# Kernel optimization log

Hardware: AMD Instinct MI355X
Metric: run time of the kernel (lower is better)

Reference implementation:

```python
import jax, jax.numpy as jnp
import numpy as np

C, H = 256, 256  # feat_num, feat_h (equirect is H x 2H)


def setup_inputs() -> dict:
    key = jax.random.key(0)
    ks = jax.random.split(key, 6)
    m = jax.random.normal(ks[0], (1, C, H, 2 * H), jnp.float32)
    b = jax.random.normal(ks[1], (1, C, H, H), jnp.float32)
    u = jax.random.normal(ks[2], (1, C, H, H), jnp.float32)
    d = jax.random.normal(ks[3], (1, C, H, H), jnp.float32)
    Wf = jax.random.normal(ks[4], (C, C, 3, 3), jnp.float32) * 0.02
    bf = jnp.zeros((C,), jnp.float32)
    Wm = jax.random.normal(ks[5], (1, 2 * C, 1, 1), jnp.float32) * 0.02
    bm = jnp.zeros((1,), jnp.float32)
    return {"m": m, "b": b, "u": u, "d": d, "Wf": Wf, "bf": bf, "Wm": Wm, "bm": bm}


def _cube2equi(cube, out_h, out_w):
    # cube: [6, C, h, h]; face order: 0 back(z-), 1 down(y-), 2 front(z+), 3 left(x-), 4 right(x+), 5 up(y+)
    h = cube.shape[-1]
    theta = (jnp.arange(out_w, dtype=cube.dtype) + 0.5) / out_w * (2.0 * jnp.pi) - jnp.pi  # longitude [-pi, pi)
    phi = jnp.pi / 2 - (jnp.arange(out_h, dtype=cube.dtype) + 0.5) / out_h * jnp.pi        # latitude [pi/2, -pi/2]
    st, ct = jnp.sin(theta)[None, :], jnp.cos(theta)[None, :]
    sp, cp = jnp.sin(phi)[:, None], jnp.cos(phi)[:, None]
    dx = cp * st
    dy = jnp.broadcast_to(sp, (out_h, out_w))
    dz = cp * ct
    ax, ay, az = jnp.abs(dx), jnp.abs(dy), jnp.abs(dz)
    mx = jnp.maximum(jnp.maximum(ax, ay), az)
    px, py, pz = dx / mx, dy / mx, dz / mx
    cond_z = (az >= ax) & (az >= ay)
    cond_x = (~cond_z) & (ax >= ay)
    face = jnp.where(cond_z, jnp.where(dz > 0, 2, 0),
           jnp.where(cond_x, jnp.where(dx > 0, 4, 3),
                              jnp.where(dy > 0, 5, 1)))
    a = jnp.where(cond_z, jnp.where(dz > 0, px, -px),
        jnp.where(cond_x, jnp.where(dx > 0, -pz, pz), px))
    bcoord = jnp.where(cond_z | cond_x, -py, jnp.where(dy > 0, pz, -pz))
    uu = jnp.clip((a + 1.0) * 0.5 * (h - 1), 0.0, h - 1)
    vv = jnp.clip((bcoord + 1.0) * 0.5 * (h - 1), 0.0, h - 1)
    u0 = jnp.floor(uu).astype(jnp.int32); v0 = jnp.floor(vv).astype(jnp.int32)
    u1 = jnp.minimum(u0 + 1, h - 1); v1 = jnp.minimum(v0 + 1, h - 1)
    wu = uu - u0; wv = vv - v0

    def samp(vi, ui):
        return cube[face, :, vi, ui]  # [out_h, out_w, C] gather over all channels

    out = (samp(v0, u0) * ((1 - wv) * (1 - wu))[..., None]
         + samp(v0, u1) * ((1 - wv) * wu)[..., None]
         + samp(v1, u0) * (wv * (1 - wu))[..., None]
         + samp(v1, u1) * (wv * wu)[..., None])
    return jnp.transpose(out, (2, 0, 1))  # [C, out_h, out_w]


def _conv(x, w, bias, pad):
    y = jax.lax.conv_general_dilated(x, w, (1, 1), [(pad, pad), (pad, pad)],
                                     dimension_numbers=("NCHW", "OIHW", "NCHW"))
    return y + bias[None, :, None, None]


def reference(m, b, u, d, Wf, bf, Wm, bm):
    h = b.shape[-1]
    empty = jnp.zeros_like(b[0])  # the torch module's zero 'emptyFace' parameter
    # faces stacked as [back, down, empty, empty, empty, up], vectorized over all channels
    cube = jnp.stack([b[0], d[0], empty, empty, empty, u[0]])  # [6, C, h, h]
    aux = _cube2equi(cube, h, 2 * h)[None]                      # [1, C, h, 2h]
    M_aux = jax.nn.relu(_conv(aux, Wf, bf, 1))
    M_main = jax.nn.relu(_conv(m, Wf, bf, 1))
    mask = jax.nn.sigmoid(_conv(jnp.concatenate([M_main, M_aux], axis=1), Wm, bm, 0))
    return m + mask * M_aux
```

## Files before the change

### kernel.cpp

```cpp
#include <hip/hip_runtime.h>
#include <hip/hip_bf16.h>

#define NPIX 131072
#define WP   514
#define XP_BYTES 67897344
#define XP_STRIDE 67962880
#define FT_BYTES 100663296

typedef __attribute__((ext_vector_type(8))) short bf16x8;
typedef __attribute__((ext_vector_type(4))) float f32x4;

typedef const __attribute__((address_space(1))) void g_cvoid;
typedef __attribute__((address_space(3))) void l_void;

__device__ __forceinline__ void async16(const void* g, void* l) {
  __builtin_amdgcn_global_load_lds((g_cvoid*)g, (l_void*)l, 16, 0, 0);
}

__global__ void zero_borders(__hip_bfloat16* Xm, __hip_bfloat16* Xa) {
  int i = blockIdx.x;
  __hip_bfloat16* X = blockIdx.y ? Xa : Xm;
  long ppix;
  if (i < 514)       ppix = i;
  else if (i < 1028) ppix = 257L * WP + (i - 514);
  else if (i < 1284) ppix = (long)(i - 1028 + 1) * WP;
  else               ppix = (long)(i - 1284 + 1) * WP + 513;
  ((unsigned int*)(X + ppix * 256))[threadIdx.x] = 0u;
}

__global__ void zero_mask(float* maskacc) {
  maskacc[blockIdx.x * 256 + threadIdx.x] = 0.f;
}

__global__ void prep_weights(const float* __restrict__ Wf, __hip_bfloat16* __restrict__ Wtt) {
  int idx = blockIdx.x * 256 + threadIdx.x;
  int cout = idx / 2304, rem = idx % 2304;
  int o = rem >> 8, ci = rem & 255;
  Wtt[(((o << 5) + (ci >> 3)) << 11) + (cout << 3) + (ci & 7)] =
      __float2bfloat16(Wf[(cout * 256 + ci) * 9 + o]);
}

__global__ void nchw_to_pad_nhwc(const float* __restrict__ src, __hip_bfloat16* __restrict__ Xp) {
  __shared__ __align__(16) __hip_bfloat16 tile[64 * 264];
  int tid = threadIdx.x;
  int p0 = blockIdx.x * 64;
  int px = tid & 63, w = tid >> 6;
  for (int k = 0; k < 64; ++k) {
    int c = (k << 2) + w;
    tile[px * 264 + c] = __float2bfloat16(src[(long)c * NPIX + p0 + px]);
  }
  __syncthreads();
  int y = p0 >> 9, x0 = p0 & 511;
  long basep = (long)(y + 1) * WP + x0 + 1;
  for (int pass = 0; pass < 8; ++pass) {
    int tpx = (pass << 3) + (tid >> 5);
    int chunk = tid & 31;
    uint4 v = *(const uint4*)&tile[tpx * 264 + (chunk << 3)];
    *(uint4*)&Xp[(basep + tpx) * 256 + (chunk << 3)] = v;
  }
}

__global__ void face_to_nhwc(const float* __restrict__ fb, const float* __restrict__ fd,
                             const float* __restrict__ fu, __hip_bfloat16* __restrict__ Ft) {
  __shared__ __align__(16) __hip_bfloat16 tile[64 * 264];
  int tid = threadIdx.x;
  int face = blockIdx.x >> 10;
  int p0 = (blockIdx.x & 1023) << 6;
  const float* src = (face == 0) ? fb : (face == 1) ? fd : fu;
  int px = tid & 63, w = tid >> 6;
  for (int k = 0; k < 64; ++k) {
    int c = (k << 2) + w;
    tile[px * 264 + c] = __float2bfloat16(src[(long)c * 65536 + p0 + px]);
  }
  __syncthreads();
  long basep = ((long)face << 16) + p0;
  for (int pass = 0; pass < 8; ++pass) {
    int tpx = (pass << 3) + (tid >> 5);
    int chunk = tid & 31;
    uint4 v = *(const uint4*)&tile[tpx * 264 + (chunk << 3)];
    *(uint4*)&Ft[((basep + tpx) << 8) + (chunk << 3)] = v;
  }
}

__device__ __forceinline__ void bf8_fma(uint4 q, float w, float* acc) {
  unsigned x;
  x = q.x; acc[0] += w * __uint_as_float(x << 16); acc[1] += w * __uint_as_float(x & 0xffff0000u);
  x = q.y; acc[2] += w * __uint_as_float(x << 16); acc[3] += w * __uint_as_float(x & 0xffff0000u);
  x = q.z; acc[4] += w * __uint_as_float(x << 16); acc[5] += w * __uint_as_float(x & 0xffff0000u);
  x = q.w; acc[6] += w * __uint_as_float(x << 16); acc[7] += w * __uint_as_float(x & 0xffff0000u);
}

__global__ void aux_gen_v2(const __hip_bfloat16* __restrict__ Ft,
                           __hip_bfloat16* __restrict__ Xp) {
  const int lane = threadIdx.x & 63;
  const int p = (blockIdx.x << 2) + (threadIdx.x >> 6);
  const int yy = p >> 9, xx = p & 511;

  float theta = ((xx + 0.5f) / 512.f) * 6.283185307179586f - 3.141592653589793f;
  float phi   = 1.5707963267948966f - ((yy + 0.5f) / 256.f) * 3.141592653589793f;
  float st = sinf(theta), ct = cosf(theta);
  float sp = sinf(phi),   cp = cosf(phi);
  float dx = cp * st, dy = sp, dz = cp * ct;
  float ax = fabsf(dx), ay = fabsf(dy), az = fabsf(dz);
  float mx = fmaxf(fmaxf(ax, ay), az);
  float pxn = dx / mx, pyn = dy / mx, pzn = dz / mx;
  bool cz = (az >= ax) && (az >= ay);
  bool cx = (!cz) && (ax >= ay);
  int face; float a, b;
  if (cz)      { face = dz > 0.f ? 2 : 0; a = dz > 0.f ? pxn : -pxn; b = -pyn; }
  else if (cx) { face = dx > 0.f ? 4 : 3; a = dx > 0.f ? -pzn : pzn; b = -pyn; }
  else         { face = dy > 0.f ? 5 : 1; a = pxn; b = dy > 0.f ? pzn : -pzn; }
  float uu = fminf(fmaxf((a + 1.f) * 0.5f * 255.f, 0.f), 255.f);
  float vv = fminf(fmaxf((b + 1.f) * 0.5f * 255.f, 0.f), 255.f);

  const long outbase = ((long)((yy + 1) * WP + xx + 1)) << 8;
  const int c0 = (lane >> 1) << 3;
  const int up = lane & 1;
  const int slot = (face == 0) ? 0 : (face == 1) ? 1 : (face == 5) ? 2 : -1;

  if (slot < 0) {
    if (!up) *(uint4*)&Xp[outbase + c0] = make_uint4(0u, 0u, 0u, 0u);
    return;
  }
  int u0 = (int)uu, v0 = (int)vv;
  int u1 = min(u0 + 1, 255), v1 = min(v0 + 1, 255);
  float wu = uu - (float)u0, wv = vv - (float)v0;
  int uc = up ? u1 : u0;
  float wA = up ? wu : (1.f - wu);
  const __hip_bfloat16* base = Ft + ((long)slot << 24);

  float acc[8] = {0.f, 0.f, 0.f, 0.f, 0.f, 0.f, 0.f, 0.f};
  uint4 q0 = *(const uint4*)&base[(((long)(v0 << 8) + uc) << 8) + c0];
  uint4 q1 = *(const uint4*)&base[(((long)(v1 << 8) + uc) << 8) + c0];
  bf8_fma(q0, (1.f - wv) * wA, acc);
  bf8_fma(q1, wv * wA, acc);
#pragma unroll
  for (int j = 0; j < 8; ++j) acc[j] += __shfl_xor(acc[j], 1);
  if (!up) {
    union { uint4 q; __hip_bfloat16 h[8]; } o;
#pragma unroll
    for (int j = 0; j < 8; ++j) o.h[j] = __float2bfloat16(acc[j]);
    *(uint4*)&Xp[outbase + c0] = o.q;
  }
}

__global__ void aux_gen(const float* __restrict__ fb, const float* __restrict__ fd,
                        const float* __restrict__ fu,
                        __hip_bfloat16* __restrict__ Xp) {
  __shared__ __align__(16) __hip_bfloat16 tile[64 * 264];
  int tid = threadIdx.x;
  int p0 = blockIdx.x * 64;
  int px = tid & 63, w = tid >> 6;

  int p = p0 + px;
  int yy = p >> 9, xx = p & 511;
  float theta = ((xx + 0.5f) / 512.f) * 6.283185307179586f - 3.141592653589793f;
  float phi   = 1.5707963267948966f - ((yy + 0.5f) / 256.f) * 3.141592653589793f;
  float st = sinf(theta), ct = cosf(theta);
  float sp = sinf(phi),   cp = cosf(phi);
  float dx = cp * st, dy = sp, dz = cp * ct;
  float ax = fabsf(dx), ay = fabsf(dy), az = fabsf(dz);
  float mx = fmaxf(fmaxf(ax, ay), az);
  float pxn = dx / mx, pyn = dy / mx, pzn = dz / mx;
  bool cz = (az >= ax) && (az >= ay);
  bool cx = (!cz) && (ax >= ay);
  int face; float a, b;
  if (cz)      { face = dz > 0.f ? 2 : 0; a = dz > 0.f ? pxn : -pxn; b = -pyn; }
  else if (cx) { face = dx > 0.f ? 4 : 3; a = dx > 0.f ? -pzn : pzn; b = -pyn; }
  else         { face = dy > 0.f ? 5 : 1; a = pxn; b = dy > 0.f ? pzn : -pzn; }
  float uu = fminf(fmaxf((a + 1.f) * 0.5f * 255.f, 0.f), 255.f);
  float vv = fminf(fmaxf((b + 1.f) * 0.5f * 255.f, 0.f), 255.f);

  const float* F = (face == 0) ? fb : (face == 1) ? fd : (face == 5) ? fu : nullptr;
  int u0 = (int)uu, v0 = (int)vv;
  int u1 = min(u0 + 1, 255), v1 = min(v0 + 1, 255);
  float wu = uu - (float)u0, wv = vv - (float)v0;
  float w00 = (1.f - wv) * (1.f - wu), w01 = (1.f - wv) * wu;
  float w10 = wv * (1.f - wu),         w11 = wv * wu;
  int i00 = v0 * 256 + u0, i01 = v0 * 256 + u1;
  int i10 = v1 * 256 + u0, i11 = v1 * 256 + u1;
  for (int k = 0; k < 64; ++k) {
    int c = (k << 2) + w;
    float val = 0.f;
    if (F) {
      const float* Fc = F + ((long)c << 16);
      val = w00 * Fc[i00] + w01 * Fc[i01] + w10 * Fc[i10] + w11 * Fc[i11];
    }
    tile[px * 264 + c] = __float2bfloat16(val);
  }
  __syncthreads();
  int y = p0 >> 9, x0g = p0 & 511;
  long basep = (long)(y + 1) * WP + x0g + 1;
  for (int pass = 0; pass < 8; ++pass) {
    int tpx = (pass << 3) + (tid >> 5);
    int chunk = tid & 31;
    uint4 v = *(const uint4*)&tile[tpx * 264 + (chunk << 3)];
    *(uint4*)&Xp[(basep + tpx) * 256 + (chunk << 3)] = v;
  }
}

__global__ __launch_bounds__(512, 4)
void conv3x3_mfma(const __hip_bfloat16* __restrict__ Xpa,
                  const __hip_bfloat16* __restrict__ Xpm,
                  const __hip_bfloat16* __restrict__ Wtt,
                  const float* __restrict__ bias,
                  const float* __restrict__ wm,
                  __hip_bfloat16* __restrict__ Out,
                  float* __restrict__ maskacc) {
  __shared__ __align__(16) __hip_bfloat16 At[4 * 80 * 32];
  const int tid = threadIdx.x;
  const int wave = tid >> 6, lane = tid & 63;
  const bool aux = (blockIdx.y == 0);
  const __hip_bfloat16* __restrict__ Xp = aux ? Xpa : Xpm;
  const float* __restrict__ wmv = aux ? wm + 256 : wm;

  const int tile = ((blockIdx.x & 7) << 7) + (blockIdx.x >> 3);
  const int x0 = (tile >> 7) << 6;
  const int y0 = (tile & 127) << 1;
  const int wrow = wave >> 2;
  const int n_off = (wave & 3) << 6;
  const int lq = lane >> 4, ln = lane & 15;

  const int srow = wave >> 1;
  const long stage_row = (long)(y0 + srow) * WP + x0;
  const int s_col = lane >> 2;
  const int s_ci  = (lane & 3) << 3;

  f32x4 acc[4][4] = {};

  for (int s = 0; s < 8; ++s) {
    const int ci0 = s << 5;
    if (wave & 1) {
      async16(Xp + ((stage_row + 48 + s_col) << 8) + ci0 + s_ci, &At[(srow * 80 + 48) << 5]);
      async16(Xp + ((stage_row + 64 + s_col) << 8) + ci0 + s_ci, &At[(srow * 80 + 64) << 5]);
    } else {
      async16(Xp + ((stage_row +  0 + s_col) << 8) + ci0 + s_ci, &At[(srow * 80 +  0) << 5]);
      async16(Xp + ((stage_row + 16 + s_col) << 8) + ci0 + s_ci, &At[(srow * 80 + 16) << 5]);
      async16(Xp + ((stage_row + 32 + s_col) << 8) + ci0 + s_ci, &At[(srow * 80 + 32) << 5]);
    }
    __syncthreads();
#pragma unroll
    for (int o = 0; o < 9; ++o) {
      const int dy = o / 3, dxo = o % 3;
      const int arow = (wrow + dy) * 80;
      bf16x8 af[4], bb[4];
#pragma unroll
      for (int mi = 0; mi < 4; ++mi)
        af[mi] = *(const bf16x8*)&At[((arow + mi * 16 + ln + dxo) << 5) + (lq << 3)];
#pragma unroll
      for (int ni = 0; ni < 4; ++ni)
        bb[ni] = *(const bf16x8*)&Wtt[(((o << 5) + (s << 2) + lq) << 11) +
                                      ((n_off + ni * 16 + ln) << 3)];
#pragma unroll
      for (int mi = 0; mi < 4; ++mi)
#pragma unroll
        for (int ni = 0; ni < 4; ++ni)
          acc[mi][ni] = __builtin_amdgcn_mfma_f32_16x16x32_bf16(af[mi], bb[ni], acc[mi][ni], 0, 0, 0);
    }
    __syncthreads();
  }

  float bv[4], wv[4];
#pragma unroll
  for (int ni = 0; ni < 4; ++ni) {
    int cc = n_off + ni * 16 + ln;
    bv[ni] = bias[cc];
    wv[ni] = wmv[cc];
  }
  const int prow = (y0 + wrow) * 512 + x0;
#pragma unroll
  for (int mi = 0; mi < 4; ++mi) {
#pragma unroll
    for (int r = 0; r < 4; ++r) {
      int pix = prow + mi * 16 + (lq << 2) + r;
      float mp = 0.f;
#pragma unroll
      for (int ni = 0; ni < 4; ++ni) {
        float v = acc[mi][ni][r] + bv[ni];
        v = v > 0.f ? v : 0.f;
        if (aux) Out[((long)pix << 8) + (n_off + ni * 16 + ln)] = __float2bfloat16(v);
        mp += v * wv[ni];
      }
      mp += __shfl_xor(mp, 1);
      mp += __shfl_xor(mp, 2);
      mp += __shfl_xor(mp, 4);
      mp += __shfl_xor(mp, 8);
      if (ln == 0) atomicAdd(&maskacc[pix], mp);
    }
  }
}

__global__ void mask_sigmoid(float* maskacc, const float* __restrict__ bm) {
  int i = blockIdx.x * 256 + threadIdx.x;
  float v = maskacc[i] + bm[0];
  maskacc[i] = 1.f / (1.f + expf(-v));
}

__global__ void final_combine(const float* __restrict__ m,
                              const __hip_bfloat16* __restrict__ MauxT,
                              const float* __restrict__ mask,
                              float* __restrict__ out) {
  __shared__ __align__(16) __hip_bfloat16 tile[64 * 264];
  __shared__ float sm[64];
  int tid = threadIdx.x;
  int p0 = blockIdx.x * 64;
  if (tid < 64) sm[tid] = mask[p0 + tid];
#pragma unroll
  for (int j = 0; j < 8; ++j) {
    int f = j * 256 + tid;
    int px = f >> 5, c8 = f & 31;
    *(uint4*)&tile[px * 264 + (c8 << 3)] =
        *(const uint4*)&MauxT[(((long)(p0 + px)) << 8) + (c8 << 3)];
  }
  __syncthreads();
  int px = tid & 63, w = tid >> 6;
  float mk = sm[px];
  for (int k = 0; k < 64; ++k) {
    int c = (k << 2) + w;
    long gi = (long)c * NPIX + p0 + px;
    out[gi] = m[gi] + mk * __bfloat162float(tile[px * 264 + c]);
  }
}

extern "C" void kernel_launch(void* const* d_in, const int* in_sizes, int n_in,
                              void* d_out, int out_size, void* d_ws, size_t ws_size,
                              hipStream_t stream) {
  const float* m  = (const float*)d_in[0];
  const float* fb = (const float*)d_in[1];
  const float* fu = (const float*)d_in[2];
  const float* fd = (const float*)d_in[3];
  const float* Wf = (const float*)d_in[4];
  const float* bf = (const float*)d_in[5];
  const float* Wm = (const float*)d_in[6];
  const float* bm = (const float*)d_in[7];
  float* out = (float*)d_out;

  char* ws = (char*)d_ws;
  const size_t NEED_FAST = (size_t)FT_BYTES + XP_STRIDE + 1179648 + 67108864 + 524288;

  if (ws_size >= NEED_FAST) {
    __hip_bfloat16* Ft     = (__hip_bfloat16*)(ws);
    __hip_bfloat16* Xp_m   = (__hip_bfloat16*)(ws);
    __hip_bfloat16* Xp_aux = (__hip_bfloat16*)(ws + (size_t)FT_BYTES);
    __hip_bfloat16* Wtt    = (__hip_bfloat16*)(ws + (size_t)FT_BYTES + XP_STRIDE);
    __hip_bfloat16* MauxT  = (__hip_bfloat16*)(ws + (size_t)FT_BYTES + XP_STRIDE + 1179648);
    float* maskacc         = (float*)(ws + (size_t)FT_BYTES + XP_STRIDE + 1179648 + 67108864);

    face_to_nhwc<<<3072, 256, 0, stream>>>(fb, fd, fu, Ft);
    aux_gen_v2<<<32768, 256, 0, stream>>>(Ft, Xp_aux);
    nchw_to_pad_nhwc<<<2048, 256, 0, stream>>>(m, Xp_m);
    zero_borders<<<dim3(1540, 2), 128, 0, stream>>>(Xp_m, Xp_aux);
    prep_weights<<<2304, 256, 0, stream>>>(Wf, Wtt);
    zero_mask<<<512, 256, 0, stream>>>(maskacc);
    conv3x3_mfma<<<dim3(1024, 2), 512, 0, stream>>>(Xp_aux, Xp_m, Wtt, bf, Wm, MauxT, maskacc);
    mask_sigmoid<<<512, 256, 0, stream>>>(maskacc, bm);
    final_combine<<<2048, 256, 0, stream>>>(m, MauxT, maskacc, out);
  } else {
    __hip_bfloat16* Xp_m   = (__hip_bfloat16*)(ws);
    __hip_bfloat16* Xp_aux = (__hip_bfloat16*)(ws + (size_t)XP_STRIDE);
    __hip_bfloat16* Wtt    = (__hip_bfloat16*)(ws + 2uL * XP_STRIDE);
    __hip_bfloat16* MauxT  = (__hip_bfloat16*)(ws + 2uL * XP_STRIDE + 1179648);
    float* maskacc         = (float*)(ws + 2uL * XP_STRIDE + 1179648 + 67108864);

    zero_borders<<<dim3(1540, 2), 128, 0, stream>>>(Xp_m, Xp_aux);
    zero_mask<<<512, 256, 0, stream>>>(maskacc);
    prep_weights<<<2304, 256, 0, stream>>>(Wf, Wtt);
    nchw_to_pad_nhwc<<<2048, 256, 0, stream>>>(m, Xp_m);
    aux_gen<<<2048, 256, 0, stream>>>(fb, fd, fu, Xp_aux);
    conv3x3_mfma<<<dim3(1024, 2), 512, 0, stream>>>(Xp_aux, Xp_m, Wtt, bf, Wm, MauxT, maskacc);
    mask_sigmoid<<<512, 256, 0, stream>>>(maskacc, bm);
    final_combine<<<2048, 256, 0, stream>>>(m, MauxT, maskacc, out);
  }
}
```

Measured before the change: 753.3 us.

## Vectorize transpose loads/stores, fuse sigmoid into combine, use fast trig

The NCHW-to-NHWC transpose kernels and final_combine now read and write float4 per thread instead of scalar floats, which cuts the number of global memory instructions. The separate mask_sigmoid kernel is removed and the sigmoid is computed inside final_combine, saving one launch and one pass over the mask buffer. Intrinsic __sinf/__cosf replace the precise trig calls in aux generation, trading a little accuracy in the sampling coordinates. The new LDS write pattern (four scattered bf16 stores per thread) may raise bank conflicts.

```diff
diff --git a/kernel.cpp b/kernel.cpp
--- a/kernel.cpp
+++ b/kernel.cpp
@@ -44,10 +44,15 @@
   __shared__ __align__(16) __hip_bfloat16 tile[64 * 264];
   int tid = threadIdx.x;
   int p0 = blockIdx.x * 64;
-  int px = tid & 63, w = tid >> 6;
-  for (int k = 0; k < 64; ++k) {
-    int c = (k << 2) + w;
-    tile[px * 264 + c] = __float2bfloat16(src[(long)c * NPIX + p0 + px]);
+  int cw = tid >> 4;
+  int px4 = (tid & 15) << 2;
+  for (int it = 0; it < 16; ++it) {
+    int c = (it << 4) + cw;
+    float4 v = *(const float4*)&src[(long)c * NPIX + p0 + px4];
+    tile[(px4 + 0) * 264 + c] = __float2bfloat16(v.x);
+    tile[(px4 + 1) * 264 + c] = __float2bfloat16(v.y);
+    tile[(px4 + 2) * 264 + c] = __float2bfloat16(v.z);
+    tile[(px4 + 3) * 264 + c] = __float2bfloat16(v.w);
   }
   __syncthreads();
   int y = p0 >> 9, x0 = p0 & 511;
@@ -67,10 +72,15 @@
   int face = blockIdx.x >> 10;
   int p0 = (blockIdx.x & 1023) << 6;
   const float* src = (face == 0) ? fb : (face == 1) ? fd : fu;
-  int px = tid & 63, w = tid >> 6;
-  for (int k = 0; k < 64; ++k) {
-    int c = (k << 2) + w;
-    tile[px * 264 + c] = __float2bfloat16(src[(long)c * 65536 + p0 + px]);
+  int cw = tid >> 4;
+  int px4 = (tid & 15) << 2;
+  for (int it = 0; it < 16; ++it) {
+    int c = (it << 4) + cw;
+    float4 v = *(const float4*)&src[(long)c * 65536 + p0 + px4];
+    tile[(px4 + 0) * 264 + c] = __float2bfloat16(v.x);
+    tile[(px4 + 1) * 264 + c] = __float2bfloat16(v.y);
+    tile[(px4 + 2) * 264 + c] = __float2bfloat16(v.z);
+    tile[(px4 + 3) * 264 + c] = __float2bfloat16(v.w);
   }
   __syncthreads();
   long basep = ((long)face << 16) + p0;
@@ -98,8 +108,8 @@
 
   float theta = ((xx + 0.5f) / 512.f) * 6.283185307179586f - 3.141592653589793f;
   float phi   = 1.5707963267948966f - ((yy + 0.5f) / 256.f) * 3.141592653589793f;
-  float st = sinf(theta), ct = cosf(theta);
-  float sp = sinf(phi),   cp = cosf(phi);
+  float st = __sinf(theta), ct = __cosf(theta);
+  float sp = __sinf(phi),   cp = __cosf(phi);
   float dx = cp * st, dy = sp, dz = cp * ct;
   float ax = fabsf(dx), ay = fabsf(dy), az = fabsf(dz);
   float mx = fmaxf(fmaxf(ax, ay), az);
@@ -156,8 +166,8 @@
   int yy = p >> 9, xx = p & 511;
   float theta = ((xx + 0.5f) / 512.f) * 6.283185307179586f - 3.141592653589793f;
   float phi   = 1.5707963267948966f - ((yy + 0.5f) / 256.f) * 3.141592653589793f;
-  float st = sinf(theta), ct = cosf(theta);
-  float sp = sinf(phi),   cp = cosf(phi);
+  float st = __sinf(theta), ct = __cosf(theta);
+  float sp = __sinf(phi),   cp = __cosf(phi);
   float dx = cp * st, dy = sp, dz = cp * ct;
   float ax = fabsf(dx), ay = fabsf(dy), az = fabsf(dz);
   float mx = fmaxf(fmaxf(ax, ay), az);
@@ -290,21 +300,19 @@
   }
 }
 
-__global__ void mask_sigmoid(float* maskacc, const float* __restrict__ bm) {
-  int i = blockIdx.x * 256 + threadIdx.x;
-  float v = maskacc[i] + bm[0];
-  maskacc[i] = 1.f / (1.f + expf(-v));
-}
-
 __global__ void final_combine(const float* __restrict__ m,
                               const __hip_bfloat16* __restrict__ MauxT,
-                              const float* __restrict__ mask,
+                              const float* __restrict__ maskacc,
+                              const float* __restrict__ bm,
                               float* __restrict__ out) {
   __shared__ __align__(16) __hip_bfloat16 tile[64 * 264];
   __shared__ float sm[64];
   int tid = threadIdx.x;
   int p0 = blockIdx.x * 64;
-  if (tid < 64) sm[tid] = mask[p0 + tid];
+  if (tid < 64) {
+    float v = maskacc[p0 + tid] + bm[0];
+    sm[tid] = 1.f / (1.f + expf(-v));
+  }
 #pragma unroll
   for (int j = 0; j < 8; ++j) {
     int f = j * 256 + tid;
@@ -313,12 +321,18 @@
         *(const uint4*)&MauxT[(((long)(p0 + px)) << 8) + (c8 << 3)];
   }
   __syncthreads();
-  int px = tid & 63, w = tid >> 6;
-  float mk = sm[px];
-  for (int k = 0; k < 64; ++k) {
-    int c = (k << 2) + w;
-    long gi = (long)c * NPIX + p0 + px;
-    out[gi] = m[gi] + mk * __bfloat162float(tile[px * 264 + c]);
+  int cw = tid >> 4;
+  int px4 = (tid & 15) << 2;
+  for (int it = 0; it < 16; ++it) {
+    int c = (it << 4) + cw;
+    long gi = (long)c * NPIX + p0 + px4;
+    float4 mv = *(const float4*)&m[gi];
+    float4 o;
+    o.x = mv.x + sm[px4 + 0] * __bfloat162float(tile[(px4 + 0) * 264 + c]);
+    o.y = mv.y + sm[px4 + 1] * __bfloat162float(tile[(px4 + 1) * 264 + c]);
+    o.z = mv.z + sm[px4 + 2] * __bfloat162float(tile[(px4 + 2) * 264 + c]);
+    o.w = mv.w + sm[px4 + 3] * __bfloat162float(tile[(px4 + 3) * 264 + c]);
+    *(float4*)&out[gi] = o;
   }
 }
 
@@ -353,8 +367,7 @@
     prep_weights<<<2304, 256, 0, stream>>>(Wf, Wtt);
     zero_mask<<<512, 256, 0, stream>>>(maskacc);
     conv3x3_mfma<<<dim3(1024, 2), 512, 0, stream>>>(Xp_aux, Xp_m, Wtt, bf, Wm, MauxT, maskacc);
-    mask_sigmoid<<<512, 256, 0, stream>>>(maskacc, bm);
-    final_combine<<<2048, 256, 0, stream>>>(m, MauxT, maskacc, out);
+    final_combine<<<2048, 256, 0, stream>>>(m, MauxT, maskacc, bm, out);
   } else {
     __hip_bfloat16* Xp_m   = (__hip_bfloat16*)(ws);
     __hip_bfloat16* Xp_aux = (__hip_bfloat16*)(ws + (size_t)XP_STRIDE);
@@ -368,7 +381,6 @@
     nchw_to_pad_nhwc<<<2048, 256, 0, stream>>>(m, Xp_m);
     aux_gen<<<2048, 256, 0, stream>>>(fb, fd, fu, Xp_aux);
     conv3x3_mfma<<<dim3(1024, 2), 512, 0, stream>>>(Xp_aux, Xp_m, Wtt, bf, Wm, MauxT, maskacc);
-    mask_sigmoid<<<512, 256, 0, stream>>>(maskacc, bm);
-    final_combine<<<2048, 256, 0, stream>>>(m, MauxT, maskacc, out);
-  }
-}
+    final_combine<<<2048, 256, 0, stream>>>(m, MauxT, maskacc, bm, out);
+  }
+}
```

After: 741.4 us. About the same (-1.6%).
